# Optimization experiments

Measured on AMD Instinct MI355X. Metric: run time of the kernel, lower is better.

The kernel has to match this reference:

```python
import jax, jax.numpy as jnp
import numpy as np

EMBED = 1024
HEADS = 16
HEAD_DIM = EMBED // HEADS
B, T = 2, 2048
ROPE_THETA = 10000.0


def _rope(x):
    # x: [B, H, T, D]; standard half-split rotary embedding, applied per head
    D = x.shape[-1]
    inv_freq = 1.0 / (ROPE_THETA ** (jnp.arange(0, D, 2, dtype=jnp.float32) / D))  # [D/2]
    freqs = jnp.arange(x.shape[2], dtype=jnp.float32)[:, None] * inv_freq[None, :]  # [T, D/2]
    cos = jnp.cos(freqs).astype(x.dtype)  # [T, D/2]
    sin = jnp.sin(freqs).astype(x.dtype)
    x1, x2 = x[..., : D // 2], x[..., D // 2 :]
    return jnp.concatenate([x1 * cos - x2 * sin, x2 * cos + x1 * sin], axis=-1)


def setup_inputs() -> dict:
    key = jax.random.key(0)
    ks = jax.random.split(key, 5)
    s = 1.0 / np.sqrt(EMBED)
    return {
        "x": jax.random.normal(ks[0], (B, T, EMBED), dtype=jnp.float32),
        "Wq": jax.random.normal(ks[1], (EMBED, EMBED), dtype=jnp.float32) * s,
        "bq": jnp.zeros((EMBED,), dtype=jnp.float32),
        "Wk": jax.random.normal(ks[2], (EMBED, EMBED), dtype=jnp.float32) * s,
        "bk": jnp.zeros((EMBED,), dtype=jnp.float32),
        "Wv": jax.random.normal(ks[3], (EMBED, EMBED), dtype=jnp.float32) * s,
        "bv": jnp.zeros((EMBED,), dtype=jnp.float32),
        "Wo": jax.random.normal(ks[4], (EMBED, EMBED), dtype=jnp.float32) * s,
        "bo": jnp.zeros((EMBED,), dtype=jnp.float32),
    }


def reference(x, Wq, bq, Wk, bk, Wv, bv, Wo, bo):
    Bb, Tt, C = x.shape
    H, D = HEADS, HEAD_DIM
    # torch Linear: y = x @ W.T + b
    def proj(W, b):
        return (jnp.einsum("btc,oc->bto", x, W) + b).reshape(Bb, Tt, H, D).transpose(0, 2, 1, 3)

    q = _rope(proj(Wq, bq))  # [B, H, T, D]
    k = _rope(proj(Wk, bk))
    v = proj(Wv, bv)
    scale = jnp.sqrt(jnp.asarray(D, dtype=x.dtype))
    scores = jnp.einsum("bhtd,bhsd->bhts", q, k) / scale  # [B, H, T, T]
    attn = jax.nn.softmax(scores, axis=-1)  # dropout = identity in eval mode
    out = jnp.einsum("bhts,bhsd->bhtd", attn, v)  # [B, H, T, D]
    out = out.transpose(0, 2, 1, 3).reshape(Bb, Tt, C)
    return jnp.einsum("btc,oc->bto", out, Wo) + bo
```

## Files before the change

kernel.cpp:

```cpp
#include <hip/hip_runtime.h>
#include <hip/hip_bf16.h>

#define EMBED 1024
#define HEADS 16
#define HDIM 64
#define BATCH 2
#define SEQ 2048
#define MTOT (BATCH*SEQ)

typedef __attribute__((ext_vector_type(2))) float f32x2;
typedef __attribute__((ext_vector_type(4))) float f32x4;
typedef __attribute__((ext_vector_type(16))) float f32x16;
typedef __attribute__((ext_vector_type(4))) short s16x4;
typedef __attribute__((ext_vector_type(8))) short bf16x8;
typedef __attribute__((ext_vector_type(4))) int i32x4;

static __device__ __forceinline__ short f2bf(float f) {
  unsigned u = __builtin_bit_cast(unsigned, f);
  unsigned r = (u + 0x7fffu + ((u >> 16) & 1u)) >> 16;
  return (short)r;
}
static __device__ __forceinline__ float bf2f(short s) {
  unsigned u = ((unsigned)(unsigned short)s) << 16;
  return __builtin_bit_cast(float, u);
}
static __device__ __forceinline__ int pack2bf(float lo, float hi) {
  unsigned ulo = __builtin_bit_cast(unsigned, lo);
  unsigned uhi = __builtin_bit_cast(unsigned, hi);
  ulo += 0x7fffu + ((ulo >> 16) & 1u);
  uhi += 0x7fffu + ((uhi >> 16) & 1u);
  return (int)__builtin_amdgcn_perm(uhi, ulo, 0x07060302u);
}
static __device__ __forceinline__ void pswap(int &a, int &b) {
  asm("v_permlane32_swap_b32 %0, %1" : "+v"(a), "+v"(b));
}

typedef __attribute__((address_space(1))) const void gvoid_t;
typedef __attribute__((address_space(3))) void lvoid_t;
static __device__ __forceinline__ void gload_lds16(const void* g, void* l) {
  __builtin_amdgcn_global_load_lds((gvoid_t*)g, (lvoid_t*)l, 16, 0, 0);
}

__global__ __launch_bounds__(256) void cvt_bf16(
    const float* __restrict__ x,
    const float* __restrict__ Wq, const float* __restrict__ Wk,
    const float* __restrict__ Wv, const float* __restrict__ Wo,
    short* __restrict__ xb,
    short* __restrict__ Wqb, short* __restrict__ Wkb,
    short* __restrict__ Wvb, short* __restrict__ Wob,
    f32x2* __restrict__ tab)
{
  int i = blockIdx.x * 256 + threadIdx.x;
  if (i >= 2097152) {
    int i2 = i - 2097152;
    int t = i2 >> 5, j = i2 & 31;
    float invf = exp2f(-(float)j * 0.4152410118609203f);
    float sn, cs;
    sincosf((float)t * invf, &sn, &cs);
    f32x2 e; e[0] = cs; e[1] = sn;
    tab[i2] = e;
    return;
  }
  const float* src; short* dst; int off;
  if (i < 1048576) { src = x; dst = xb; off = i; }
  else {
    int j = i - 1048576;
    int w = j >> 18; off = j & 262143;
    src = (w == 0) ? Wq : (w == 1) ? Wk : (w == 2) ? Wv : Wo;
    dst = (w == 0) ? Wqb : (w == 1) ? Wkb : (w == 2) ? Wvb : Wob;
  }
  f32x4 v = ((const f32x4*)src)[off];
  s16x4 h;
#pragma unroll
  for (int j = 0; j < 4; ++j) h[j] = f2bf(v[j]);
  ((s16x4*)dst)[off] = h;
}

__global__ __launch_bounds__(256) void qkv_gemm(
    const short* __restrict__ xb,
    const short* __restrict__ Wqb, const short* __restrict__ Wkb, const short* __restrict__ Wvb,
    const float* __restrict__ bq, const float* __restrict__ bk, const float* __restrict__ bv,
    const f32x2* __restrict__ tab,
    short* __restrict__ Qb, short* __restrict__ Kb, short* __restrict__ Vb)
{
  __shared__ short As[128][32];
  __shared__ short Bs[128][32];
  int tid = threadIdx.x;
  int lane = tid & 63, wid = tid >> 6;
  int wm = wid >> 1, wn = wid & 1;
  int bid = blockIdx.x;
  int lg = (bid & 7) * 96 + (bid >> 3);
  int bm = lg / 24;
  int bncol = lg % 24;
  int wsel = bncol >> 3, bnn = bncol & 7;
  const short* W    = (wsel == 0) ? Wqb : (wsel == 1) ? Wkb : Wvb;
  const float* bias = (wsel == 0) ? bq : (wsel == 1) ? bk : bv;

  f32x4 acc[4][4] = {};

  const short* Abase = xb + (size_t)bm * 128 * EMBED;
  const short* Bbase = W + (size_t)bnn * 128 * EMBED;
  int grow = tid >> 2;
  int gcol = (tid & 3) * 8;
  char* AsB = (char*)&As[0][0];
  char* BsB = (char*)&Bs[0][0];

  for (int kt = 0; kt < EMBED / 32; ++kt) {
#pragma unroll
    for (int i = 0; i < 2; ++i) {
      gload_lds16(&Abase[(size_t)(i * 64 + grow) * EMBED + kt * 32 + gcol],
                  AsB + i * 4096 + wid * 1024);
      gload_lds16(&Bbase[(size_t)(i * 64 + grow) * EMBED + kt * 32 + gcol],
                  BsB + i * 4096 + wid * 1024);
    }
    __syncthreads();
    bf16x8 af[4], bfr[4];
#pragma unroll
    for (int mf = 0; mf < 4; ++mf)
      af[mf] = *(const bf16x8*)&As[wm * 64 + mf * 16 + (lane & 15)][(lane >> 4) * 8];
#pragma unroll
    for (int nf = 0; nf < 4; ++nf)
      bfr[nf] = *(const bf16x8*)&Bs[wn * 64 + nf * 16 + (lane & 15)][(lane >> 4) * 8];
    if (wsel == 2) {
#pragma unroll
      for (int mf = 0; mf < 4; ++mf)
#pragma unroll
        for (int nf = 0; nf < 4; ++nf)
          acc[mf][nf] = __builtin_amdgcn_mfma_f32_16x16x32_bf16(bfr[mf], af[nf], acc[mf][nf], 0, 0, 0);
    } else {
#pragma unroll
      for (int mf = 0; mf < 4; ++mf)
#pragma unroll
        for (int nf = 0; nf < 4; ++nf)
          acc[mf][nf] = __builtin_amdgcn_mfma_f32_16x16x32_bf16(af[mf], bfr[nf], acc[mf][nf], 0, 0, 0);
    }
    __syncthreads();
  }

  if (wsel < 2) {
    short* dst = (wsel == 0) ? Qb : Kb;
    float sc = (wsel == 0) ? 0.18033688011112042f : 1.0f;
#pragma unroll
    for (int nf = 0; nf < 2; ++nf) {
      int col = bnn * 128 + wn * 64 + nf * 16 + (lane & 15);
      int h = col >> 6, j = col & 31;
      float b1 = bias[col], b2 = bias[col + 32];
#pragma unroll
      for (int mf = 0; mf < 4; ++mf) {
        int row0 = bm * 128 + wm * 64 + mf * 16 + ((lane >> 4) << 2);
#pragma unroll
        for (int r = 0; r < 4; ++r) {
          int m = row0 + r;
          int b_ = m >> 11, t = m & (SEQ - 1);
          f32x2 e = tab[t * 32 + j];
          float a1 = acc[mf][nf][r] + b1;
          float a2 = acc[mf][nf + 2][r] + b2;
          size_t o = (((size_t)(b_ * HEADS + h)) * SEQ + t) * HDIM + j;
          dst[o]      = f2bf((a1 * e[0] - a2 * e[1]) * sc);
          dst[o + 32] = f2bf((a2 * e[0] + a1 * e[1]) * sc);
        }
      }
    }
  } else {
#pragma unroll
    for (int mf = 0; mf < 4; ++mf) {
#pragma unroll
      for (int r = 0; r < 4; ++r) {
        int cch = bnn * 128 + wn * 64 + mf * 16 + ((lane >> 4) << 2) + r;
        int h = cch >> 6, d = cch & 63;
        float bb = bias[cch];
#pragma unroll
        for (int nf = 0; nf < 4; ++nf) {
          int m = bm * 128 + wm * 64 + nf * 16 + (lane & 15);
          int b_ = m >> 11, t = m & (SEQ - 1);
          Vb[((size_t)(b_ * HEADS + h) * HDIM + d) * SEQ + t] = f2bf(acc[mf][nf][r] + bb);
        }
      }
    }
  }
}

#define QBLK 128
#define KBLK 128

__global__ __launch_bounds__(256, 2) void attn_kernel(
    const short* __restrict__ Qb, const short* __restrict__ Kb,
    const short* __restrict__ Vb, short* __restrict__ Ob)
{
  __shared__ short Ks[KBLK][68];
  __shared__ short Vs[HDIM][132];

  int tid = threadIdx.x, lane = tid & 63, wid = tid >> 6;
  int l31 = lane & 31, lhi = lane >> 5;

  int bid = blockIdx.x;
  int swz = (bid & 7) * 64 + (bid >> 3);
  int qi = swz & 15, bh = swz >> 4;
  int b = bh >> 4, h = bh & 15;

  const short* Qp = Qb + ((size_t)bh * SEQ + qi * QBLK + wid * 32) * HDIM;
  const short* Kp = Kb + (size_t)bh * SEQ * HDIM;
  const short* Vp = Vb + (size_t)bh * HDIM * SEQ;

  bf16x8 qf[4];
#pragma unroll
  for (int cc = 0; cc < 4; ++cc)
    qf[cc] = *(const bf16x8*)&Qp[(size_t)l31 * HDIM + cc * 16 + lhi * 8];

  f32x16 oacc0 = {}, oacc1 = {}, lacc = {};
  bf16x8 vones;
#pragma unroll
  for (int j = 0; j < 8; ++j) vones[j] = (short)0x3F80;

  bf16x8 kreg[4], vreg[4];
#pragma unroll
  for (int i = 0; i < 4; ++i) {
    int s = tid + i * 256;
    kreg[i] = *(const bf16x8*)&Kp[(size_t)(s >> 3) * HDIM + (s & 7) * 8];
    vreg[i] = *(const bf16x8*)&Vp[(size_t)(s >> 4) * SEQ + (s & 15) * 8];
  }

  for (int kt = 0; kt < SEQ / KBLK; ++kt) {
#pragma unroll
    for (int i = 0; i < 4; ++i) {
      int s = tid + i * 256;
      *(bf16x8*)&Ks[s >> 3][(s & 7) * 8] = kreg[i];
      *(bf16x8*)&Vs[s >> 4][(s & 15) * 8] = vreg[i];
    }
    __syncthreads();

    if (kt + 1 < SEQ / KBLK) {
#pragma unroll
      for (int i = 0; i < 4; ++i) {
        int s = tid + i * 256;
        kreg[i] = *(const bf16x8*)&Kp[(size_t)((kt + 1) * KBLK + (s >> 3)) * HDIM + (s & 7) * 8];
        vreg[i] = *(const bf16x8*)&Vp[(size_t)(s >> 4) * SEQ + (kt + 1) * KBLK + (s & 15) * 8];
      }
    }

#pragma unroll
    for (int kb = 0; kb < 4; ++kb) {
      f32x16 sA = {}, sB = {};
      {
        bf16x8 a0 = *(const bf16x8*)&Ks[kb * 32 + l31][0 * 16 + lhi * 8];
        bf16x8 a1 = *(const bf16x8*)&Ks[kb * 32 + l31][1 * 16 + lhi * 8];
        bf16x8 a2 = *(const bf16x8*)&Ks[kb * 32 + l31][2 * 16 + lhi * 8];
        bf16x8 a3 = *(const bf16x8*)&Ks[kb * 32 + l31][3 * 16 + lhi * 8];
        sA = __builtin_amdgcn_mfma_f32_32x32x16_bf16(a0, qf[0], sA, 0, 0, 0);
        sB = __builtin_amdgcn_mfma_f32_32x32x16_bf16(a1, qf[1], sB, 0, 0, 0);
        sA = __builtin_amdgcn_mfma_f32_32x32x16_bf16(a2, qf[2], sA, 0, 0, 0);
        sB = __builtin_amdgcn_mfma_f32_32x32x16_bf16(a3, qf[3], sB, 0, 0, 0);
      }
      f32x16 p;
#pragma unroll
      for (int i = 0; i < 16; ++i)
        p[i] = __builtin_amdgcn_exp2f(sA[i] + sB[i]);

#pragma unroll
      for (int c = 0; c < 2; ++c) {
        int w0 = pack2bf(p[8 * c + 0], p[8 * c + 1]);
        int w1 = pack2bf(p[8 * c + 2], p[8 * c + 3]);
        int w2 = pack2bf(p[8 * c + 4], p[8 * c + 5]);
        int w3 = pack2bf(p[8 * c + 6], p[8 * c + 7]);
        pswap(w0, w2);
        pswap(w1, w3);
        i32x4 pw; pw[0] = w0; pw[1] = w1; pw[2] = w2; pw[3] = w3;
        bf16x8 pa = __builtin_bit_cast(bf16x8, pw);

        bf16x8 vf0 = *(const bf16x8*)&Vs[l31][kb * 32 + c * 16 + lhi * 8];
        bf16x8 vf1 = *(const bf16x8*)&Vs[32 + l31][kb * 32 + c * 16 + lhi * 8];
        lacc = __builtin_amdgcn_mfma_f32_32x32x16_bf16(pa, vones, lacc, 0, 0, 0);
        oacc0 = __builtin_amdgcn_mfma_f32_32x32x16_bf16(pa, vf0, oacc0, 0, 0, 0);
        oacc1 = __builtin_amdgcn_mfma_f32_32x32x16_bf16(pa, vf1, oacc1, 0, 0, 0);
      }
    }
    __syncthreads();
  }

#pragma unroll
  for (int r = 0; r < 16; ++r) {
    int qrow = (r & 3) + 8 * (r >> 2) + 4 * lhi;
    int t = qi * QBLK + wid * 32 + qrow;
    float inv = 1.0f / lacc[r];
    size_t base = ((size_t)(b * SEQ + t)) * EMBED + h * HDIM;
    Ob[base + l31]      = f2bf(oacc0[r] * inv);
    Ob[base + 32 + l31] = f2bf(oacc1[r] * inv);
  }
}

__global__ __launch_bounds__(256) void out_gemm(
    const short* __restrict__ A, const short* __restrict__ Wob,
    const float* __restrict__ bo, float* __restrict__ C)
{
  __shared__ short As[128][32];
  __shared__ short Bs[128][32];
  int tid = threadIdx.x;
  int lane = tid & 63, wid = tid >> 6;
  int wm = wid >> 1, wn = wid & 1;
  int bid = blockIdx.x;
  int lg = (bid & 7) * 32 + (bid >> 3);
  int bm = lg >> 3, bn = lg & 7;

  f32x4 acc[4][4] = {};
  const short* Abase = A + (size_t)bm * 128 * EMBED;
  const short* Bbase = Wob + (size_t)bn * 128 * EMBED;
  int grow = tid >> 2;
  int gcol = (tid & 3) * 8;
  char* AsB = (char*)&As[0][0];
  char* BsB = (char*)&Bs[0][0];

  for (int kt = 0; kt < EMBED / 32; ++kt) {
#pragma unroll
    for (int i = 0; i < 2; ++i) {
      gload_lds16(&Abase[(size_t)(i * 64 + grow) * EMBED + kt * 32 + gcol],
                  AsB + i * 4096 + wid * 1024);
      gload_lds16(&Bbase[(size_t)(i * 64 + grow) * EMBED + kt * 32 + gcol],
                  BsB + i * 4096 + wid * 1024);
    }
    __syncthreads();
    bf16x8 af[4], bfr[4];
#pragma unroll
    for (int mf = 0; mf < 4; ++mf)
      af[mf] = *(const bf16x8*)&As[wm * 64 + mf * 16 + (lane & 15)][(lane >> 4) * 8];
#pragma unroll
    for (int nf = 0; nf < 4; ++nf)
      bfr[nf] = *(const bf16x8*)&Bs[wn * 64 + nf * 16 + (lane & 15)][(lane >> 4) * 8];
#pragma unroll
    for (int mf = 0; mf < 4; ++mf)
#pragma unroll
      for (int nf = 0; nf < 4; ++nf)
        acc[mf][nf] = __builtin_amdgcn_mfma_f32_16x16x32_bf16(af[mf], bfr[nf], acc[mf][nf], 0, 0, 0);
    __syncthreads();
  }

#pragma unroll
  for (int nf = 0; nf < 4; ++nf) {
    int col = bn * 128 + wn * 64 + nf * 16 + (lane & 15);
    float bb = bo[col];
#pragma unroll
    for (int mf = 0; mf < 4; ++mf) {
      int row0 = bm * 128 + wm * 64 + mf * 16 + ((lane >> 4) << 2);
#pragma unroll
      for (int r = 0; r < 4; ++r)
        C[(size_t)(row0 + r) * EMBED + col] = acc[mf][nf][r] + bb;
    }
  }
}

extern "C" void kernel_launch(void* const* d_in, const int* in_sizes, int n_in,
                              void* d_out, int out_size, void* d_ws, size_t ws_size,
                              hipStream_t stream) {
  const float* x  = (const float*)d_in[0];
  const float* Wq = (const float*)d_in[1];
  const float* bq = (const float*)d_in[2];
  const float* Wk = (const float*)d_in[3];
  const float* bk = (const float*)d_in[4];
  const float* Wv = (const float*)d_in[5];
  const float* bv = (const float*)d_in[6];
  const float* Wo = (const float*)d_in[7];
  const float* bo = (const float*)d_in[8];
  float* out = (float*)d_out;
  char* ws = (char*)d_ws;

  const size_t MB = 1u << 20;
  short* Qb  = (short*)(ws);
  short* Kb  = (short*)(ws + 8 * MB);
  short* Vb  = (short*)(ws + 16 * MB);
  short* XOb = (short*)(ws + 24 * MB);
  short* Wqb = (short*)(ws + 32 * MB);
  short* Wkb = (short*)(ws + 34 * MB);
  short* Wvb = (short*)(ws + 36 * MB);
  short* Wob = (short*)(ws + 38 * MB);
  f32x2* tab = (f32x2*)(ws + 40 * MB);

  cvt_bf16<<<dim3(8448), dim3(256), 0, stream>>>(x, Wq, Wk, Wv, Wo, XOb, Wqb, Wkb, Wvb, Wob, tab);
  qkv_gemm<<<dim3(32 * 24), dim3(256), 0, stream>>>(XOb, Wqb, Wkb, Wvb, bq, bk, bv, tab, Qb, Kb, Vb);
  attn_kernel<<<dim3(BATCH * HEADS * (SEQ / QBLK)), dim3(256), 0, stream>>>(Qb, Kb, Vb, XOb);
  out_gemm<<<dim3(32 * 8), dim3(256), 0, stream>>>(XOb, Wob, bo, out);
}
```

Measured before the change: 137.6 us.

## Deepen GEMM K-tiles with XOR-swizzled LDS and restructure attention score/pack loop

Both projection GEMMs now stage 64-wide K tiles instead of 32, halving the barrier count, and use an XOR swizzle on the LDS layout to avoid bank conflicts on fragment reads. The grouped block-index remapping is removed in favor of plain row-major block order. The attention inner loop computes two 32-key score tiles at once, dropping the split-accumulator add, and packs probabilities to bf16 with the hardware v_cvt_pk_bf16_f32 instruction after a rounding bias. Risks are lost L2 locality from removing the tile swizzle, higher register pressure, and slightly different rounding on ties.

```diff
diff --git a/kernel.cpp b/kernel.cpp
--- a/kernel.cpp
+++ b/kernel.cpp
@@ -24,12 +24,13 @@
   unsigned u = ((unsigned)(unsigned short)s) << 16;
   return __builtin_bit_cast(float, u);
 }
-static __device__ __forceinline__ int pack2bf(float lo, float hi) {
-  unsigned ulo = __builtin_bit_cast(unsigned, lo);
-  unsigned uhi = __builtin_bit_cast(unsigned, hi);
-  ulo += 0x7fffu + ((ulo >> 16) & 1u);
-  uhi += 0x7fffu + ((uhi >> 16) & 1u);
-  return (int)__builtin_amdgcn_perm(uhi, ulo, 0x07060302u);
+static __device__ __forceinline__ int pack2bf_fast(float lo, float hi) {
+  unsigned ulo = __builtin_bit_cast(unsigned, lo) + 0x8000u;
+  unsigned uhi = __builtin_bit_cast(unsigned, hi) + 0x8000u;
+  int r;
+  asm("v_cvt_pk_bf16_f32 %0, %1, %2" : "=v"(r)
+      : "v"(__builtin_bit_cast(float, ulo)), "v"(__builtin_bit_cast(float, uhi)));
+  return r;
 }
 static __device__ __forceinline__ void pswap(int &a, int &b) {
   asm("v_permlane32_swap_b32 %0, %1" : "+v"(a), "+v"(b));
@@ -83,15 +84,13 @@
     const f32x2* __restrict__ tab,
     short* __restrict__ Qb, short* __restrict__ Kb, short* __restrict__ Vb)
 {
-  __shared__ short As[128][32];
-  __shared__ short Bs[128][32];
+  __shared__ short As[128][64];
+  __shared__ short Bs[128][64];
   int tid = threadIdx.x;
   int lane = tid & 63, wid = tid >> 6;
   int wm = wid >> 1, wn = wid & 1;
-  int bid = blockIdx.x;
-  int lg = (bid & 7) * 96 + (bid >> 3);
-  int bm = lg / 24;
-  int bncol = lg % 24;
+  int bm = blockIdx.x / 24;
+  int bncol = blockIdx.x % 24;
   int wsel = bncol >> 3, bnn = bncol & 7;
   const short* W    = (wsel == 0) ? Wqb : (wsel == 1) ? Wkb : Wvb;
   const float* bias = (wsel == 0) ? bq : (wsel == 1) ? bk : bv;
@@ -100,39 +99,44 @@
 
   const short* Abase = xb + (size_t)bm * 128 * EMBED;
   const short* Bbase = W + (size_t)bnn * 128 * EMBED;
-  int grow = tid >> 2;
-  int gcol = (tid & 3) * 8;
   char* AsB = (char*)&As[0][0];
   char* BsB = (char*)&Bs[0][0];
 
-  for (int kt = 0; kt < EMBED / 32; ++kt) {
-#pragma unroll
-    for (int i = 0; i < 2; ++i) {
-      gload_lds16(&Abase[(size_t)(i * 64 + grow) * EMBED + kt * 32 + gcol],
-                  AsB + i * 4096 + wid * 1024);
-      gload_lds16(&Bbase[(size_t)(i * 64 + grow) * EMBED + kt * 32 + gcol],
-                  BsB + i * 4096 + wid * 1024);
-    }
-    __syncthreads();
-    bf16x8 af[4], bfr[4];
-#pragma unroll
-    for (int mf = 0; mf < 4; ++mf)
-      af[mf] = *(const bf16x8*)&As[wm * 64 + mf * 16 + (lane & 15)][(lane >> 4) * 8];
-#pragma unroll
-    for (int nf = 0; nf < 4; ++nf)
-      bfr[nf] = *(const bf16x8*)&Bs[wn * 64 + nf * 16 + (lane & 15)][(lane >> 4) * 8];
-    if (wsel == 2) {
+  for (int kt = 0; kt < EMBED / 64; ++kt) {
+#pragma unroll
+    for (int i = 0; i < 4; ++i) {
+      int s = tid + i * 256;
+      int row = s >> 3, c = s & 7;
+      int cs = c ^ (row & 7);
+      gload_lds16(&Abase[(size_t)row * EMBED + kt * 64 + cs * 8],
+                  AsB + i * 4096 + wid * 1024 + lane * 16);
+      gload_lds16(&Bbase[(size_t)row * EMBED + kt * 64 + cs * 8],
+                  BsB + i * 4096 + wid * 1024 + lane * 16);
+    }
+    __syncthreads();
+#pragma unroll
+    for (int kk = 0; kk < 2; ++kk) {
+      int cp = ((kk * 4 + (lane >> 4)) ^ (lane & 7)) * 8;
+      bf16x8 af[4], bfr[4];
 #pragma unroll
       for (int mf = 0; mf < 4; ++mf)
-#pragma unroll
-        for (int nf = 0; nf < 4; ++nf)
-          acc[mf][nf] = __builtin_amdgcn_mfma_f32_16x16x32_bf16(bfr[mf], af[nf], acc[mf][nf], 0, 0, 0);
-    } else {
-#pragma unroll
-      for (int mf = 0; mf < 4; ++mf)
-#pragma unroll
-        for (int nf = 0; nf < 4; ++nf)
-          acc[mf][nf] = __builtin_amdgcn_mfma_f32_16x16x32_bf16(af[mf], bfr[nf], acc[mf][nf], 0, 0, 0);
+        af[mf] = *(const bf16x8*)&As[wm * 64 + mf * 16 + (lane & 15)][cp];
+#pragma unroll
+      for (int nf = 0; nf < 4; ++nf)
+        bfr[nf] = *(const bf16x8*)&Bs[wn * 64 + nf * 16 + (lane & 15)][cp];
+      if (wsel == 2) {
+#pragma unroll
+        for (int mf = 0; mf < 4; ++mf)
+#pragma unroll
+          for (int nf = 0; nf < 4; ++nf)
+            acc[mf][nf] = __builtin_amdgcn_mfma_f32_16x16x32_bf16(bfr[mf], af[nf], acc[mf][nf], 0, 0, 0);
+      } else {
+#pragma unroll
+        for (int mf = 0; mf < 4; ++mf)
+#pragma unroll
+          for (int nf = 0; nf < 4; ++nf)
+            acc[mf][nf] = __builtin_amdgcn_mfma_f32_16x16x32_bf16(af[mf], bfr[nf], acc[mf][nf], 0, 0, 0);
+      }
     }
     __syncthreads();
   }
@@ -239,36 +243,52 @@
     }
 
 #pragma unroll
-    for (int kb = 0; kb < 4; ++kb) {
-      f32x16 sA = {}, sB = {};
-      {
-        bf16x8 a0 = *(const bf16x8*)&Ks[kb * 32 + l31][0 * 16 + lhi * 8];
-        bf16x8 a1 = *(const bf16x8*)&Ks[kb * 32 + l31][1 * 16 + lhi * 8];
-        bf16x8 a2 = *(const bf16x8*)&Ks[kb * 32 + l31][2 * 16 + lhi * 8];
-        bf16x8 a3 = *(const bf16x8*)&Ks[kb * 32 + l31][3 * 16 + lhi * 8];
-        sA = __builtin_amdgcn_mfma_f32_32x32x16_bf16(a0, qf[0], sA, 0, 0, 0);
-        sB = __builtin_amdgcn_mfma_f32_32x32x16_bf16(a1, qf[1], sB, 0, 0, 0);
-        sA = __builtin_amdgcn_mfma_f32_32x32x16_bf16(a2, qf[2], sA, 0, 0, 0);
-        sB = __builtin_amdgcn_mfma_f32_32x32x16_bf16(a3, qf[3], sB, 0, 0, 0);
-      }
-      f32x16 p;
-#pragma unroll
-      for (int i = 0; i < 16; ++i)
-        p[i] = __builtin_amdgcn_exp2f(sA[i] + sB[i]);
+    for (int kbp = 0; kbp < 4; kbp += 2) {
+      f32x16 s0 = {}, s1 = {};
+#pragma unroll
+      for (int cc = 0; cc < 4; ++cc) {
+        bf16x8 a0 = *(const bf16x8*)&Ks[(kbp + 0) * 32 + l31][cc * 16 + lhi * 8];
+        bf16x8 a1 = *(const bf16x8*)&Ks[(kbp + 1) * 32 + l31][cc * 16 + lhi * 8];
+        s0 = __builtin_amdgcn_mfma_f32_32x32x16_bf16(a0, qf[cc], s0, 0, 0, 0);
+        s1 = __builtin_amdgcn_mfma_f32_32x32x16_bf16(a1, qf[cc], s1, 0, 0, 0);
+      }
+      f32x16 p0, p1;
+#pragma unroll
+      for (int i = 0; i < 16; ++i) {
+        p0[i] = __builtin_amdgcn_exp2f(s0[i]);
+        p1[i] = __builtin_amdgcn_exp2f(s1[i]);
+      }
 
 #pragma unroll
       for (int c = 0; c < 2; ++c) {
-        int w0 = pack2bf(p[8 * c + 0], p[8 * c + 1]);
-        int w1 = pack2bf(p[8 * c + 2], p[8 * c + 3]);
-        int w2 = pack2bf(p[8 * c + 4], p[8 * c + 5]);
-        int w3 = pack2bf(p[8 * c + 6], p[8 * c + 7]);
+        int w0 = pack2bf_fast(p0[8 * c + 0], p0[8 * c + 1]);
+        int w1 = pack2bf_fast(p0[8 * c + 2], p0[8 * c + 3]);
+        int w2 = pack2bf_fast(p0[8 * c + 4], p0[8 * c + 5]);
+        int w3 = pack2bf_fast(p0[8 * c + 6], p0[8 * c + 7]);
         pswap(w0, w2);
         pswap(w1, w3);
         i32x4 pw; pw[0] = w0; pw[1] = w1; pw[2] = w2; pw[3] = w3;
         bf16x8 pa = __builtin_bit_cast(bf16x8, pw);
 
-        bf16x8 vf0 = *(const bf16x8*)&Vs[l31][kb * 32 + c * 16 + lhi * 8];
-        bf16x8 vf1 = *(const bf16x8*)&Vs[32 + l31][kb * 32 + c * 16 + lhi * 8];
+        bf16x8 vf0 = *(const bf16x8*)&Vs[l31][(kbp + 0) * 32 + c * 16 + lhi * 8];
+        bf16x8 vf1 = *(const bf16x8*)&Vs[32 + l31][(kbp + 0) * 32 + c * 16 + lhi * 8];
+        lacc = __builtin_amdgcn_mfma_f32_32x32x16_bf16(pa, vones, lacc, 0, 0, 0);
+        oacc0 = __builtin_amdgcn_mfma_f32_32x32x16_bf16(pa, vf0, oacc0, 0, 0, 0);
+        oacc1 = __builtin_amdgcn_mfma_f32_32x32x16_bf16(pa, vf1, oacc1, 0, 0, 0);
+      }
+#pragma unroll
+      for (int c = 0; c < 2; ++c) {
+        int w0 = pack2bf_fast(p1[8 * c + 0], p1[8 * c + 1]);
+        int w1 = pack2bf_fast(p1[8 * c + 2], p1[8 * c + 3]);
+        int w2 = pack2bf_fast(p1[8 * c + 4], p1[8 * c + 5]);
+        int w3 = pack2bf_fast(p1[8 * c + 6], p1[8 * c + 7]);
+        pswap(w0, w2);
+        pswap(w1, w3);
+        i32x4 pw; pw[0] = w0; pw[1] = w1; pw[2] = w2; pw[3] = w3;
+        bf16x8 pa = __builtin_bit_cast(bf16x8, pw);
+
+        bf16x8 vf0 = *(const bf16x8*)&Vs[l31][(kbp + 1) * 32 + c * 16 + lhi * 8];
+        bf16x8 vf1 = *(const bf16x8*)&Vs[32 + l31][(kbp + 1) * 32 + c * 16 + lhi * 8];
         lacc = __builtin_amdgcn_mfma_f32_32x32x16_bf16(pa, vones, lacc, 0, 0, 0);
         oacc0 = __builtin_amdgcn_mfma_f32_32x32x16_bf16(pa, vf0, oacc0, 0, 0, 0);
         oacc1 = __builtin_amdgcn_mfma_f32_32x32x16_bf16(pa, vf1, oacc1, 0, 0, 0);
@@ -292,44 +312,47 @@
     const short* __restrict__ A, const short* __restrict__ Wob,
     const float* __restrict__ bo, float* __restrict__ C)
 {
-  __shared__ short As[128][32];
-  __shared__ short Bs[128][32];
+  __shared__ short As[128][64];
+  __shared__ short Bs[128][64];
   int tid = threadIdx.x;
   int lane = tid & 63, wid = tid >> 6;
   int wm = wid >> 1, wn = wid & 1;
-  int bid = blockIdx.x;
-  int lg = (bid & 7) * 32 + (bid >> 3);
-  int bm = lg >> 3, bn = lg & 7;
+  int bm = blockIdx.x >> 3, bn = blockIdx.x & 7;
 
   f32x4 acc[4][4] = {};
   const short* Abase = A + (size_t)bm * 128 * EMBED;
   const short* Bbase = Wob + (size_t)bn * 128 * EMBED;
-  int grow = tid >> 2;
-  int gcol = (tid & 3) * 8;
   char* AsB = (char*)&As[0][0];
   char* BsB = (char*)&Bs[0][0];
 
-  for (int kt = 0; kt < EMBED / 32; ++kt) {
-#pragma unroll
-    for (int i = 0; i < 2; ++i) {
-      gload_lds16(&Abase[(size_t)(i * 64 + grow) * EMBED + kt * 32 + gcol],
-                  AsB + i * 4096 + wid * 1024);
-      gload_lds16(&Bbase[(size_t)(i * 64 + grow) * EMBED + kt * 32 + gcol],
-                  BsB + i * 4096 + wid * 1024);
-    }
-    __syncthreads();
-    bf16x8 af[4], bfr[4];
-#pragma unroll
-    for (int mf = 0; mf < 4; ++mf)
-      af[mf] = *(const bf16x8*)&As[wm * 64 + mf * 16 + (lane & 15)][(lane >> 4) * 8];
-#pragma unroll
-    for (int nf = 0; nf < 4; ++nf)
-      bfr[nf] = *(const bf16x8*)&Bs[wn * 64 + nf * 16 + (lane & 15)][(lane >> 4) * 8];
-#pragma unroll
-    for (int mf = 0; mf < 4; ++mf)
+  for (int kt = 0; kt < EMBED / 64; ++kt) {
+#pragma unroll
+    for (int i = 0; i < 4; ++i) {
+      int s = tid + i * 256;
+      int row = s >> 3, c = s & 7;
+      int cs = c ^ (row & 7);
+      gload_lds16(&Abase[(size_t)row * EMBED + kt * 64 + cs * 8],
+                  AsB + i * 4096 + wid * 1024 + lane * 16);
+      gload_lds16(&Bbase[(size_t)row * EMBED + kt * 64 + cs * 8],
+                  BsB + i * 4096 + wid * 1024 + lane * 16);
+    }
+    __syncthreads();
+#pragma unroll
+    for (int kk = 0; kk < 2; ++kk) {
+      int cp = ((kk * 4 + (lane >> 4)) ^ (lane & 7)) * 8;
+      bf16x8 af[4], bfr[4];
+#pragma unroll
+      for (int mf = 0; mf < 4; ++mf)
+        af[mf] = *(const bf16x8*)&As[wm * 64 + mf * 16 + (lane & 15)][cp];
 #pragma unroll
       for (int nf = 0; nf < 4; ++nf)
-        acc[mf][nf] = __builtin_amdgcn_mfma_f32_16x16x32_bf16(af[mf], bfr[nf], acc[mf][nf], 0, 0, 0);
+        bfr[nf] = *(const bf16x8*)&Bs[wn * 64 + nf * 16 + (lane & 15)][cp];
+#pragma unroll
+      for (int mf = 0; mf < 4; ++mf)
+#pragma unroll
+        for (int nf = 0; nf < 4; ++nf)
+          acc[mf][nf] = __builtin_amdgcn_mfma_f32_16x16x32_bf16(af[mf], bfr[nf], acc[mf][nf], 0, 0, 0);
+    }
     __syncthreads();
   }
 
```

Measured after the change: 121.7 us. -11.6%, faster.
